# Kernel tuning notes

Hardware: AMD Instinct MI355X
Metric: run time of the kernel (lower is better)

The kernel has to match this reference:

```python
import jax, jax.numpy as jnp
import numpy as np
import math

# Model dims (see shape_source)
BATCH, SEQ, HH, WW = 32, 128, 32, 32   # x: (B, seq_len, H, W); L = H*W = 1024
D_MODEL = 1024                          # hidden_dim
N2 = 4                                  # n=8 -> 4 complex S4D modes
L_MAX = 64                              # SSM kernel length (l_max)


def _layernorm(x, gamma, beta, eps=1e-5):
    mu = jnp.mean(x, axis=-1, keepdims=True)
    var = jnp.var(x, axis=-1, keepdims=True)
    return (x - mu) * jax.lax.rsqrt(var + eps) * gamma + beta


def setup_inputs() -> dict:
    key = jax.random.key(0)
    ks = jax.random.split(key, 12)
    d_in = SEQ  # d_input = d_output = seq_len
    inp = {
        "x": jax.random.normal(ks[0], (BATCH, SEQ, HH, WW), dtype=jnp.float32),
        # encoder Linear(d_input -> d_model)
        "W_enc": jax.random.normal(ks[1], (d_in, D_MODEL), dtype=jnp.float32) / math.sqrt(d_in),
        "b_enc": jnp.zeros((D_MODEL,), dtype=jnp.float32),
        # S4D SSM parameters (per d_model channel, N2 complex modes)
        "log_dt": (jax.random.uniform(ks[2], (D_MODEL,), dtype=jnp.float32)
                   * (math.log(0.1) - math.log(0.001)) + math.log(0.001)),
        "A_log_real": jnp.full((D_MODEL, N2), math.log(0.5), dtype=jnp.float32),
        "A_imag": jnp.broadcast_to(math.pi * jnp.arange(N2, dtype=jnp.float32), (D_MODEL, N2)).copy(),
        "C_real": jax.random.normal(ks[3], (D_MODEL, N2), dtype=jnp.float32) * 0.5,
        "C_imag": jax.random.normal(ks[4], (D_MODEL, N2), dtype=jnp.float32) * 0.5,
        "D": jax.random.normal(ks[5], (D_MODEL,), dtype=jnp.float32),
        # position-wise GLU mixing Linear(d_model -> 2*d_model)
        "W_glu": jax.random.normal(ks[6], (D_MODEL, 2 * D_MODEL), dtype=jnp.float32) / math.sqrt(D_MODEL),
        "b_glu": jnp.zeros((2 * D_MODEL,), dtype=jnp.float32),
        "ln_gamma": jnp.ones((D_MODEL,), dtype=jnp.float32),
        "ln_beta": jnp.zeros((D_MODEL,), dtype=jnp.float32),
        # decoder Linear(d_model -> d_output)
        "W_dec": jax.random.normal(ks[7], (D_MODEL, d_in), dtype=jnp.float32) / math.sqrt(D_MODEL),
        "b_dec": jnp.zeros((d_in,), dtype=jnp.float32),
    }
    return inp


def reference(x, W_enc, b_enc, log_dt, A_log_real, A_imag, C_real, C_imag, D,
              W_glu, b_glu, ln_gamma, ln_beta, W_dec, b_dec):
    Bsz, S, Hh, Ww = x.shape
    L = Hh * Ww
    u = x.reshape(Bsz, S, L)                                  # (B, d_input, L)
    # encoder applied per position along L
    h = jnp.einsum('bdl,de->ble', u, W_enc) + b_enc           # (B, L, d_model)

    # ---- S4D kernel (ZOH discretization, B=1, diagonal A) ----
    dt = jnp.exp(log_dt)                                      # (d,)
    A = -jnp.exp(A_log_real) + 1j * A_imag                    # (d, n2) complex
    Cc = C_real + 1j * C_imag
    dtA = A * dt[:, None]                                     # (d, n2)
    Bd = (jnp.exp(dtA) - 1.0) / A                             # ZOH input matrix
    t = jnp.arange(L_MAX)
    vand = jnp.exp(dtA[:, :, None] * t)                       # (d, n2, l_max)
    K = 2.0 * jnp.einsum('dn,dnl->dl', Cc * Bd, vand).real    # (d, l_max)

    # ---- causal FFT convolution along L + skip D*u ----
    z = jnp.swapaxes(h, 1, 2)                                 # (B, d, L)
    n_fft = L + L_MAX
    y = jnp.fft.irfft(jnp.fft.rfft(z, n=n_fft) * jnp.fft.rfft(K, n=n_fft), n=n_fft)[..., :L]
    y = y + D[:, None] * z                                    # (B, d, L)

    # ---- block: GELU -> GLU mixing -> residual -> LayerNorm ----
    y = jax.nn.gelu(jnp.swapaxes(y, 1, 2))                    # (B, L, d)
    g = y @ W_glu + b_glu                                     # (B, L, 2d)
    g = g[..., :D_MODEL] * jax.nn.sigmoid(g[..., D_MODEL:])
    h = _layernorm(h + g, ln_gamma, ln_beta)                  # (B, L, d)

    out = h @ W_dec + b_dec                                   # (B, L, d_output)
    out = jnp.swapaxes(out, 1, 2).reshape(Bsz, S, Hh, Ww)
    return out
```

## Files before the change

kernel.cpp:

```cpp
#include <hip/hip_runtime.h>
#include <hip/hip_bf16.h>
#include <math.h>

#define B_ 32
#define S_ 128
#define L_ 1024
#define D_ 1024

typedef unsigned short u16;
typedef __attribute__((ext_vector_type(8))) __bf16 bf16x8;
typedef __attribute__((ext_vector_type(4))) float f32x4;

__device__ __forceinline__ float bf2f(u16 u) {
    return __uint_as_float(((unsigned)u) << 16);
}
__device__ __forceinline__ u16 f2bf(float f) {
    unsigned u = __float_as_uint(f);
    u += 0x7FFF + ((u >> 16) & 1);
    return (u16)(u >> 16);
}
__device__ __forceinline__ float gelu_tanh(float x) {
    float x3 = x * x * x;
    float t = tanhf(0.7978845608028654f * (x + 0.044715f * x3));
    return 0.5f * x * (1.0f + t);
}
__device__ __forceinline__ float sigmoidf(float x) {
    return 1.0f / (1.0f + expf(-x));
}
__device__ __forceinline__ void gld16(const void* g, void* l) {
    __builtin_amdgcn_global_load_lds((const __attribute__((address_space(1))) void*)g,
                                     (__attribute__((address_space(3))) void*)l, 16, 0, 0);
}

__global__ __launch_bounds__(256) void k_ssmk(
        const float* __restrict__ log_dt, const float* __restrict__ Alr,
        const float* __restrict__ Aim, const float* __restrict__ Cr,
        const float* __restrict__ Ci, float* __restrict__ Kt) {
    int tid = blockIdx.x * 256 + threadIdx.x;
    int d = tid & (D_ - 1);
    int j = tid >> 10;
    float dt = expf(log_dt[d]);
    float acc = 0.f;
    #pragma unroll
    for (int n = 0; n < 4; ++n) {
        float ar = -expf(Alr[d * 4 + n]);
        float ai = Aim[d * 4 + n];
        float wr = ar * dt, wi = ai * dt;
        float ew = expf(wr);
        float sw, cw; sincosf(wi, &sw, &cw);
        float ur = ew * cw - 1.0f, ui = ew * sw;
        float inv = 1.0f / (ar * ar + ai * ai);
        float bdr = (ur * ar + ui * ai) * inv;
        float bdi = (ui * ar - ur * ai) * inv;
        float cr = Cr[d * 4 + n], ci = Ci[d * 4 + n];
        float cbr = cr * bdr - ci * bdi;
        float cbi = cr * bdi + ci * bdr;
        float ej = expf(wr * (float)j);
        float sj, cj; sincosf(wi * (float)j, &sj, &cj);
        acc += 2.0f * ej * (cbr * cj - cbi * sj);
    }
    Kt[j * D_ + d] = acc;
}

__global__ __launch_bounds__(256) void k_tcast(
        const float* __restrict__ src0, u16* __restrict__ dst0, int R, int C) {
    __shared__ float tile[64][65];
    const float* src = src0 + (size_t)blockIdx.z * R * C;
    u16* dst = dst0 + (size_t)blockIdx.z * R * C;
    int c0 = blockIdx.x * 64;
    int r0 = blockIdx.y * 64;
    int t = threadIdx.x;
    #pragma unroll
    for (int p = 0; p < 4; ++p) {
        int fid = p * 256 + t;
        int rr = fid >> 4, cc = (fid & 15) * 4;
        float4 v = *(const float4*)&src[(size_t)(r0 + rr) * C + c0 + cc];
        tile[rr][cc + 0] = v.x; tile[rr][cc + 1] = v.y;
        tile[rr][cc + 2] = v.z; tile[rr][cc + 3] = v.w;
    }
    __syncthreads();
    #pragma unroll
    for (int p = 0; p < 4; ++p) {
        int fid = p * 256 + t;
        int rr = fid >> 4, cc = (fid & 15) * 4;
        ushort4 o;
        o.x = f2bf(tile[cc + 0][rr]);
        o.y = f2bf(tile[cc + 1][rr]);
        o.z = f2bf(tile[cc + 2][rr]);
        o.w = f2bf(tile[cc + 3][rr]);
        *(ushort4*)&dst[(size_t)(c0 + rr) * R + r0 + cc] = o;
    }
}

__global__ __launch_bounds__(256) void k_enc_mfma(
        const u16* __restrict__ xb, const u16* __restrict__ WeT,
        const float* __restrict__ be, u16* __restrict__ hb) {
    __shared__ u16 As[128 * 128];
    __shared__ u16 Bs[128 * 128];
    int t = threadIdx.x;
    int lane = t & 63, wid = t >> 6;
    int wr = wid & 1, wc = wid >> 1;
    int orig = blockIdx.x;
    int wgid = (orig & 7) * 256 + (orig >> 3);
    int m0 = (wgid >> 3) * 128;
    int e0 = (wgid & 7) * 128;

    #pragma unroll
    for (int c = 0; c < 8; ++c) {
        int ch = wid * 8 + c;
        int r = ch * 4 + (lane >> 4);
        int g = (lane & 15) ^ (r & 15);
        gld16(&xb[(size_t)(m0 + r) * 128 + g * 8], &As[ch * 512]);
        gld16(&WeT[(size_t)(e0 + r) * 128 + g * 8], &Bs[ch * 512]);
    }
    int co4[4];
    #pragma unroll
    for (int kh = 0; kh < 4; ++kh)
        co4[kh] = ((((lane >> 4) + kh * 4) ^ (lane & 15)) * 8);
    int arow[4], brow[4];
    #pragma unroll
    for (int i = 0; i < 4; ++i) arow[i] = (wr * 64 + i * 16 + (lane & 15)) * 128;
    #pragma unroll
    for (int q = 0; q < 4; ++q) brow[q] = (wc * 64 + q * 16 + (lane & 15)) * 128;

    __syncthreads();
    f32x4 acc[4][4] = {};
    #pragma unroll
    for (int kh = 0; kh < 4; ++kh) {
        bf16x8 af[4], bfr[4];
        #pragma unroll
        for (int i = 0; i < 4; ++i) af[i] = *(const bf16x8*)&As[arow[i] + co4[kh]];
        #pragma unroll
        for (int q = 0; q < 4; ++q) bfr[q] = *(const bf16x8*)&Bs[brow[q] + co4[kh]];
        __builtin_amdgcn_s_setprio(1);
        #pragma unroll
        for (int i = 0; i < 4; ++i)
            #pragma unroll
            for (int q = 0; q < 4; ++q)
                acc[i][q] = __builtin_amdgcn_mfma_f32_16x16x32_bf16(af[i], bfr[q], acc[i][q], 0, 0, 0);
        __builtin_amdgcn_s_setprio(0);
    }
    #pragma unroll
    for (int q = 0; q < 4; ++q) {
        int e = e0 + wc * 64 + q * 16 + (lane & 15);
        float bias = be[e];
        #pragma unroll
        for (int i = 0; i < 4; ++i) {
            #pragma unroll
            for (int r = 0; r < 4; ++r) {
                int m = m0 + wr * 64 + i * 16 + (lane >> 4) * 4 + r;
                hb[(size_t)m * 1024 + e] = f2bf(acc[i][q][r] + bias);
            }
        }
    }
}

__global__ __launch_bounds__(256) void k_conv(
        const u16* __restrict__ hb, const float* __restrict__ Kt,
        const float* __restrict__ Dv, u16* __restrict__ yg) {
    __shared__ float hs[128][64];
    int b = blockIdx.z;
    int l0 = blockIdx.y * 64;
    int d0 = blockIdx.x * 64;
    int t = threadIdx.x;
    int dl = t & 63, lg = t >> 6;
    #pragma unroll
    for (int p = 0; p < 8; ++p) {
        int fid = p * 256 + t;
        int r = fid >> 4, c4 = fid & 15;
        int l = l0 - 64 + r;
        float4 v = make_float4(0.f, 0.f, 0.f, 0.f);
        if (l >= 0) {
            ushort4 u = *(const ushort4*)&hb[((size_t)b * 1024 + l) * 1024 + d0 + c4 * 4];
            v = make_float4(bf2f(u.x), bf2f(u.y), bf2f(u.z), bf2f(u.w));
        }
        *(float4*)&hs[r][c4 * 4] = v;
    }
    float kr[64];
    #pragma unroll
    for (int j = 0; j < 64; ++j) kr[j] = Kt[j * 1024 + d0 + dl];
    float Dd = Dv[d0 + dl];
    __syncthreads();
    float acc[16] = {};
    int rbase = lg * 16 + 1;
    #pragma unroll
    for (int s = 0; s < 15; ++s) {
        float hv = hs[rbase + s][dl];
        #pragma unroll
        for (int i = 0; i <= 14; ++i)
            if (i <= s) acc[i] = fmaf(kr[i + 63 - s], hv, acc[i]);
    }
    #pragma unroll
    for (int s = 15; s < 64; ++s) {
        float hv = hs[rbase + s][dl];
        #pragma unroll
        for (int i = 0; i < 16; ++i)
            acc[i] = fmaf(kr[i + 63 - s], hv, acc[i]);
    }
    #pragma unroll
    for (int s = 64; s < 79; ++s) {
        float hv = hs[rbase + s][dl];
        #pragma unroll
        for (int i = 1; i < 16; ++i)
            if (i >= s - 63) acc[i] = fmaf(kr[i + 63 - s], hv, acc[i]);
    }
    #pragma unroll
    for (int i = 0; i < 16; ++i) {
        int l = l0 + lg * 16 + i;
        float z = hs[64 + lg * 16 + i][dl];
        float y = acc[i] + Dd * z;
        yg[((size_t)b * 1024 + l) * 1024 + d0 + dl] = f2bf(gelu_tanh(y));
    }
}

__global__ __launch_bounds__(512, 2) void k_glu256(
        const u16* __restrict__ yg, const u16* __restrict__ WgT,
        const float* __restrict__ bg, u16* __restrict__ hb) {
    __shared__ u16 Asm[2][16384];
    __shared__ u16 Bsm[2][16384];
    int t = threadIdx.x;
    int lane = t & 63, wid = t >> 6;
    int wr = wid >> 2, wc = wid & 3;

    int orig = blockIdx.x;
    int wgid = (orig & 7) * 128 + (orig >> 3);
    int m0 = (wgid >> 3) * 256;
    int p0g = (wgid & 7) * 128;

    int rl = lane >> 3;
    int gsw = ((lane & 7) ^ rl) * 8;
    int ch0 = wid * 2, ch1 = wid * 2 + 1;
    int rA0 = (ch0 >> 3) * 128 + (ch0 & 7) * 8 + rl;
    int rA1 = (ch1 >> 3) * 128 + (ch1 & 7) * 8 + rl;
    int dA0 = ((ch0 >> 3) * 128 + (ch0 & 7) * 8) * 64;
    int dA1 = ((ch1 >> 3) * 128 + (ch1 & 7) * 8) * 64;
    int rB0 = (ch0 >> 2) * 64 + (ch0 & 3) * 8 + rl;
    int rB1 = (ch1 >> 2) * 64 + (ch1 & 3) * 8 + rl;
    int dB0 = ((ch0 >> 2) * 64 + (ch0 & 3) * 8) * 64;
    int dB1 = ((ch1 >> 2) * 64 + (ch1 & 3) * 8) * 64;
    int gB0 = ((rB0 >> 4) & 1) * 1024 + p0g + (((rB0 >> 5) << 4) | (rB0 & 15));
    int gB1 = ((rB1 >> 4) & 1) * 1024 + p0g + (((rB1 >> 5) << 4) | (rB1 & 15));

    int co0 = (((lane >> 4) + 0) ^ (lane & 7)) * 8;
    int co1 = (((lane >> 4) + 4) ^ (lane & 7)) * 8;
    int abase = (wr * 128 + (lane & 15)) * 64;
    int bbase = (wc * 64 + (lane & 15)) * 64;

#define STG_A0(BUF, K0) { gld16(&yg[(size_t)(m0 + rA0) * 1024 + (K0) + gsw], &Asm[BUF][dA0]); \
                          gld16(&yg[(size_t)(m0 + rA1) * 1024 + (K0) + gsw], &Asm[BUF][dA1]); }
#define STG_A1(BUF, K0) { gld16(&yg[(size_t)(m0 + rA0 + 64) * 1024 + (K0) + gsw], &Asm[BUF][dA0 + 4096]); \
                          gld16(&yg[(size_t)(m0 + rA1 + 64) * 1024 + (K0) + gsw], &Asm[BUF][dA1 + 4096]); }
#define STG_B0(BUF, K0) { gld16(&WgT[(size_t)gB0 * 1024 + (K0) + gsw], &Bsm[BUF][dB0]); \
                          gld16(&WgT[(size_t)gB1 * 1024 + (K0) + gsw], &Bsm[BUF][dB1]); }
#define STG_B1(BUF, K0) { gld16(&WgT[(size_t)(gB0 + 16) * 1024 + (K0) + gsw], &Bsm[BUF][dB0 + 2048]); \
                          gld16(&WgT[(size_t)(gB1 + 16) * 1024 + (K0) + gsw], &Bsm[BUF][dB1 + 2048]); }
#define RD_A(MH) { _Pragma("unroll") for (int i = 0; i < 4; ++i) { \
        a0[i][0] = *(const bf16x8*)&Ac[abase + (MH) * 4096 + i * 1024 + co0]; \
        a0[i][1] = *(const bf16x8*)&Ac[abase + (MH) * 4096 + i * 1024 + co1]; } }
#define RD_B(BB, OFS) { _Pragma("unroll") for (int q = 0; q < 2; ++q) { \
        BB[q][0] = *(const bf16x8*)&Bc[bbase + (OFS) + q * 1024 + co0]; \
        BB[q][1] = *(const bf16x8*)&Bc[bbase + (OFS) + q * 1024 + co1]; } }
#define MFMA_CL(MI, BB, NQ) { __builtin_amdgcn_s_setprio(1); \
    _Pragma("unroll") for (int i = 0; i < 4; ++i) \
        _Pragma("unroll") for (int q = 0; q < 2; ++q) { \
            acc[(MI) * 4 + i][(NQ) + q] = __builtin_amdgcn_mfma_f32_16x16x32_bf16(a0[i][0], BB[q][0], acc[(MI) * 4 + i][(NQ) + q], 0, 0, 0); \
            acc[(MI) * 4 + i][(NQ) + q] = __builtin_amdgcn_mfma_f32_16x16x32_bf16(a0[i][1], BB[q][1], acc[(MI) * 4 + i][(NQ) + q], 0, 0, 0); } \
    __builtin_amdgcn_s_setprio(0); }

    f32x4 acc[8][4] = {};
    bf16x8 a0[4][2], b0[2][2], b1[2][2];

    STG_A0(0, 0); STG_B0(0, 0); STG_B1(0, 0); STG_A1(0, 0);

    int cur = 0;
    for (int kt = 0; kt < 15; ++kt) {
        const u16* Ac = &Asm[cur][0];
        const u16* Bc = &Bsm[cur][0];
        int nxt = cur ^ 1, k1 = (kt + 1) * 64;
        asm volatile("s_waitcnt vmcnt(2)" ::: "memory");
        __builtin_amdgcn_s_barrier();
        RD_A(0); RD_B(b0, 0);
        STG_A0(nxt, k1);
        __builtin_amdgcn_s_barrier();
        MFMA_CL(0, b0, 0);
        RD_B(b1, 2048);
        STG_B0(nxt, k1);
        __builtin_amdgcn_s_barrier();
        MFMA_CL(0, b1, 2);
        asm volatile("s_waitcnt vmcnt(4)" ::: "memory");
        __builtin_amdgcn_s_barrier();
        RD_A(1);
        STG_B1(nxt, k1);
        __builtin_amdgcn_s_barrier();
        MFMA_CL(1, b0, 0);
        STG_A1(nxt, k1);
        __builtin_amdgcn_s_barrier();
        MFMA_CL(1, b1, 2);
        cur = nxt;
    }
    {
        const u16* Ac = &Asm[cur][0];
        const u16* Bc = &Bsm[cur][0];
        asm volatile("s_waitcnt vmcnt(2)" ::: "memory");
        __builtin_amdgcn_s_barrier();
        RD_A(0); RD_B(b0, 0);
        MFMA_CL(0, b0, 0);
        RD_B(b1, 2048);
        MFMA_CL(0, b1, 2);
        asm volatile("s_waitcnt vmcnt(0)" ::: "memory");
        __builtin_amdgcn_s_barrier();
        RD_A(1);
        MFMA_CL(1, b0, 0);
        MFMA_CL(1, b1, 2);
    }
    #pragma unroll
    for (int i = 0; i < 8; ++i) {
        #pragma unroll
        for (int tt = 0; tt < 2; ++tt) {
            int col = p0g + (wc * 2 + tt) * 16 + (lane & 15);
            float b1v = bg[col];
            float b2v = bg[1024 + col];
            #pragma unroll
            for (int r = 0; r < 4; ++r) {
                int m = m0 + wr * 128 + i * 16 + (lane >> 4) * 4 + r;
                size_t idx = (size_t)m * 1024 + col;
                float g1 = acc[i][tt * 2][r] + b1v;
                float g2 = acc[i][tt * 2 + 1][r] + b2v;
                hb[idx] = f2bf(bf2f(hb[idx]) + g1 * sigmoidf(g2));
            }
        }
    }
#undef STG_A0
#undef STG_A1
#undef STG_B0
#undef STG_B1
#undef RD_A
#undef RD_B
#undef MFMA_CL
}

__global__ __launch_bounds__(256) void k_ln(
        u16* __restrict__ hb, const float* __restrict__ gamma,
        const float* __restrict__ beta) {
    int row = blockIdx.x;
    int t = threadIdx.x;
    size_t base = (size_t)row * 1024;
    ushort4 u = *(const ushort4*)&hb[base + t * 4];
    float v0 = bf2f(u.x), v1 = bf2f(u.y), v2 = bf2f(u.z), v3 = bf2f(u.w);
    float s = v0 + v1 + v2 + v3;
    float s2 = v0 * v0 + v1 * v1 + v2 * v2 + v3 * v3;
    #pragma unroll
    for (int off = 32; off > 0; off >>= 1) {
        s += __shfl_down(s, off);
        s2 += __shfl_down(s2, off);
    }
    __shared__ float rs[4], rs2[4];
    int wid = t >> 6, lane = t & 63;
    if (lane == 0) { rs[wid] = s; rs2[wid] = s2; }
    __syncthreads();
    float ts = rs[0] + rs[1] + rs[2] + rs[3];
    float ts2 = rs2[0] + rs2[1] + rs2[2] + rs2[3];
    float mean = ts * (1.0f / 1024.0f);
    float var = ts2 * (1.0f / 1024.0f) - mean * mean;
    float rstd = rsqrtf(var + 1e-5f);
    float4 gm = *(const float4*)&gamma[t * 4];
    float4 bt = *(const float4*)&beta[t * 4];
    ushort4 o;
    o.x = f2bf((v0 - mean) * rstd * gm.x + bt.x);
    o.y = f2bf((v1 - mean) * rstd * gm.y + bt.y);
    o.z = f2bf((v2 - mean) * rstd * gm.z + bt.z);
    o.w = f2bf((v3 - mean) * rstd * gm.w + bt.w);
    *(ushort4*)&hb[base + t * 4] = o;
}

__global__ __launch_bounds__(256) void k_dec_mfma(
        const u16* __restrict__ hb, const u16* __restrict__ WdT,
        const float* __restrict__ bd, float* __restrict__ out) {
    __shared__ __align__(16) char smem[65536];
    u16* As = (u16*)smem;
    u16* Bs = (u16*)(smem + 32768);
    float* Ts = (float*)smem;
    int t = threadIdx.x;
    int lane = t & 63, wid = t >> 6;
    int wr = wid & 1, wc = wid >> 1;
    int m0 = blockIdx.x * 128;
    int bb = m0 >> 10, l0 = m0 & 1023;

    int gsrc = (((lane & 7) ^ (lane >> 3)) * 8);
    int rr4[4];
    #pragma unroll
    for (int c = 0; c < 4; ++c) rr4[c] = (wid * 4 + c) * 8 + (lane >> 3);
    int co[2];
    co[0] = (((lane >> 4) + 0) ^ (lane & 7)) * 8;
    co[1] = (((lane >> 4) + 4) ^ (lane & 7)) * 8;
    int arow[4], brow[4];
    #pragma unroll
    for (int i = 0; i < 4; ++i) arow[i] = (wr * 64 + i * 16 + (lane & 15)) * 64;
    #pragma unroll
    for (int q = 0; q < 4; ++q) brow[q] = (wc * 64 + q * 16 + (lane & 15)) * 64;

    f32x4 acc[4][4] = {};
    #pragma unroll
    for (int c = 0; c < 4; ++c) {
        int ch = wid * 4 + c;
        gld16(&hb[(size_t)(m0 + rr4[c]) * 1024 + gsrc], &As[0 * 8192 + ch * 512]);
        gld16(&WdT[(size_t)rr4[c] * 1024 + gsrc], &Bs[0 * 8192 + ch * 512]);
    }
    __syncthreads();
    int cur = 0;
    for (int kt = 0; kt < 16; ++kt) {
        if (kt < 15) {
            int k0 = (kt + 1) * 64;
            #pragma unroll
            for (int c = 0; c < 4; ++c) {
                int ch = wid * 4 + c;
                gld16(&hb[(size_t)(m0 + rr4[c]) * 1024 + k0 + gsrc], &As[(cur ^ 1) * 8192 + ch * 512]);
                gld16(&WdT[(size_t)rr4[c] * 1024 + k0 + gsrc], &Bs[(cur ^ 1) * 8192 + ch * 512]);
            }
        }
        #pragma unroll
        for (int kh = 0; kh < 2; ++kh) {
            bf16x8 af[4], bfr[4];
            #pragma unroll
            for (int i = 0; i < 4; ++i) af[i] = *(const bf16x8*)&As[cur * 8192 + arow[i] + co[kh]];
            #pragma unroll
            for (int q = 0; q < 4; ++q) bfr[q] = *(const bf16x8*)&Bs[cur * 8192 + brow[q] + co[kh]];
            __builtin_amdgcn_s_setprio(1);
            #pragma unroll
            for (int i = 0; i < 4; ++i)
                #pragma unroll
                for (int q = 0; q < 4; ++q)
                    acc[i][q] = __builtin_amdgcn_mfma_f32_16x16x32_bf16(af[i], bfr[q], acc[i][q], 0, 0, 0);
            __builtin_amdgcn_s_setprio(0);
        }
        __syncthreads();
        cur ^= 1;
    }
    __syncthreads();
    #pragma unroll
    for (int ro = 0; ro < 2; ++ro) {
        if (wc == ro) {
            #pragma unroll
            for (int i = 0; i < 4; ++i)
                #pragma unroll
                for (int q = 0; q < 4; ++q) {
                    int sl = q * 16 + (lane & 15);
                    float bias = bd[ro * 64 + sl];
                    #pragma unroll
                    for (int r = 0; r < 4; ++r) {
                        int ml = wr * 64 + i * 16 + (lane >> 4) * 4 + r;
                        Ts[sl * 132 + ml] = acc[i][q][r] + bias;
                    }
                }
        }
        __syncthreads();
        #pragma unroll
        for (int p = 0; p < 8; ++p) {
            int fid = p * 256 + t;
            int sl = fid >> 5, c = (fid & 31) * 4;
            float4 v = *(const float4*)&Ts[sl * 132 + c];
            *(float4*)&out[(size_t)bb * 131072 + (size_t)(ro * 64 + sl) * 1024 + l0 + c] = v;
        }
        __syncthreads();
    }
}

extern "C" void kernel_launch(void* const* d_in, const int* in_sizes, int n_in,
                              void* d_out, int out_size, void* d_ws, size_t ws_size,
                              hipStream_t stream) {
    (void)in_sizes; (void)n_in; (void)out_size; (void)ws_size;
    const float* x   = (const float*)d_in[0];
    const float* We  = (const float*)d_in[1];
    const float* be  = (const float*)d_in[2];
    const float* ldt = (const float*)d_in[3];
    const float* Alr = (const float*)d_in[4];
    const float* Aim = (const float*)d_in[5];
    const float* Cr  = (const float*)d_in[6];
    const float* Ci  = (const float*)d_in[7];
    const float* Dv  = (const float*)d_in[8];
    const float* Wg  = (const float*)d_in[9];
    const float* bg  = (const float*)d_in[10];
    const float* gam = (const float*)d_in[11];
    const float* bet = (const float*)d_in[12];
    const float* Wd  = (const float*)d_in[13];
    const float* bd  = (const float*)d_in[14];
    float* out = (float*)d_out;

    u16* hb = (u16*)d_ws;
    u16* yg = hb + 33554432ull;
    float* Kt = (float*)(yg + 33554432ull);
    u16* WgT = (u16*)(Kt + 65536);
    u16* WdT = WgT + 2097152ull;
    u16* WeT = WdT + 131072ull;
    u16* xb  = yg;

    k_tcast<<<dim3(32, 16, 1), 256, 0, stream>>>(Wg, WgT, 1024, 2048);
    k_tcast<<<dim3(2, 16, 1), 256, 0, stream>>>(Wd, WdT, 1024, 128);
    k_tcast<<<dim3(16, 2, 1), 256, 0, stream>>>(We, WeT, 128, 1024);
    k_tcast<<<dim3(16, 2, 32), 256, 0, stream>>>(x, xb, 128, 1024);
    k_ssmk<<<256, 256, 0, stream>>>(ldt, Alr, Aim, Cr, Ci, Kt);
    k_enc_mfma<<<2048, 256, 0, stream>>>(xb, WeT, be, hb);
    k_conv<<<dim3(16, 16, 32), 256, 0, stream>>>(hb, Kt, Dv, yg);
    k_glu256<<<1024, 512, 0, stream>>>(yg, WgT, bg, hb);
    k_ln<<<32768, 256, 0, stream>>>(hb, gam, bet);
    k_dec_mfma<<<256, 256, 0, stream>>>(hb, WdT, bd, out);
}
```

Baseline: 343.8 us.

## Restructure GLU GEMM mainloop into a 4-stage K=32 LDS pipeline

```diff
diff --git a/kernel.cpp b/kernel.cpp
--- a/kernel.cpp
+++ b/kernel.cpp
@@ -216,8 +216,8 @@
 __global__ __launch_bounds__(512, 2) void k_glu256(
         const u16* __restrict__ yg, const u16* __restrict__ WgT,
         const float* __restrict__ bg, u16* __restrict__ hb) {
-    __shared__ u16 Asm[2][16384];
-    __shared__ u16 Bsm[2][16384];
+    __shared__ u16 Asm[4][8192];
+    __shared__ u16 Bsm[4][8192];
     int t = threadIdx.x;
     int lane = t & 63, wid = t >> 6;
     int wr = wid >> 2, wc = wid & 3;
@@ -227,92 +227,60 @@
     int m0 = (wgid >> 3) * 256;
     int p0g = (wgid & 7) * 128;
 
-    int rl = lane >> 3;
-    int gsw = ((lane & 7) ^ rl) * 8;
-    int ch0 = wid * 2, ch1 = wid * 2 + 1;
-    int rA0 = (ch0 >> 3) * 128 + (ch0 & 7) * 8 + rl;
-    int rA1 = (ch1 >> 3) * 128 + (ch1 & 7) * 8 + rl;
-    int dA0 = ((ch0 >> 3) * 128 + (ch0 & 7) * 8) * 64;
-    int dA1 = ((ch1 >> 3) * 128 + (ch1 & 7) * 8) * 64;
-    int rB0 = (ch0 >> 2) * 64 + (ch0 & 3) * 8 + rl;
-    int rB1 = (ch1 >> 2) * 64 + (ch1 & 3) * 8 + rl;
-    int dB0 = ((ch0 >> 2) * 64 + (ch0 & 3) * 8) * 64;
-    int dB1 = ((ch1 >> 2) * 64 + (ch1 & 3) * 8) * 64;
-    int gB0 = ((rB0 >> 4) & 1) * 1024 + p0g + (((rB0 >> 5) << 4) | (rB0 & 15));
-    int gB1 = ((rB1 >> 4) & 1) * 1024 + p0g + (((rB1 >> 5) << 4) | (rB1 & 15));
-
-    int co0 = (((lane >> 4) + 0) ^ (lane & 7)) * 8;
-    int co1 = (((lane >> 4) + 4) ^ (lane & 7)) * 8;
-    int abase = (wr * 128 + (lane & 15)) * 64;
-    int bbase = (wc * 64 + (lane & 15)) * 64;
-
-#define STG_A0(BUF, K0) { gld16(&yg[(size_t)(m0 + rA0) * 1024 + (K0) + gsw], &Asm[BUF][dA0]); \
-                          gld16(&yg[(size_t)(m0 + rA1) * 1024 + (K0) + gsw], &Asm[BUF][dA1]); }
-#define STG_A1(BUF, K0) { gld16(&yg[(size_t)(m0 + rA0 + 64) * 1024 + (K0) + gsw], &Asm[BUF][dA0 + 4096]); \
-                          gld16(&yg[(size_t)(m0 + rA1 + 64) * 1024 + (K0) + gsw], &Asm[BUF][dA1 + 4096]); }
-#define STG_B0(BUF, K0) { gld16(&WgT[(size_t)gB0 * 1024 + (K0) + gsw], &Bsm[BUF][dB0]); \
-                          gld16(&WgT[(size_t)gB1 * 1024 + (K0) + gsw], &Bsm[BUF][dB1]); }
-#define STG_B1(BUF, K0) { gld16(&WgT[(size_t)(gB0 + 16) * 1024 + (K0) + gsw], &Bsm[BUF][dB0 + 2048]); \
-                          gld16(&WgT[(size_t)(gB1 + 16) * 1024 + (K0) + gsw], &Bsm[BUF][dB1 + 2048]); }
-#define RD_A(MH) { _Pragma("unroll") for (int i = 0; i < 4; ++i) { \
-        a0[i][0] = *(const bf16x8*)&Ac[abase + (MH) * 4096 + i * 1024 + co0]; \
-        a0[i][1] = *(const bf16x8*)&Ac[abase + (MH) * 4096 + i * 1024 + co1]; } }
-#define RD_B(BB, OFS) { _Pragma("unroll") for (int q = 0; q < 2; ++q) { \
-        BB[q][0] = *(const bf16x8*)&Bc[bbase + (OFS) + q * 1024 + co0]; \
-        BB[q][1] = *(const bf16x8*)&Bc[bbase + (OFS) + q * 1024 + co1]; } }
-#define MFMA_CL(MI, BB, NQ) { __builtin_amdgcn_s_setprio(1); \
+    int crow = lane >> 2;
+    int gofs = (((lane & 3) ^ ((lane >> 3) & 3)) * 8);
+    int ch0 = wid * 2, ch1 = ch0 + 1;
+    int rA0 = ch0 * 16 + crow, rA1 = ch1 * 16 + crow;
+    int dA0 = ch0 * 512, dA1 = ch1 * 512;
+    int gB0 = ((rA0 >> 4) & 1) * 1024 + p0g + (((rA0 >> 5) << 4) | (rA0 & 15));
+    int gB1 = ((rA1 >> 4) & 1) * 1024 + p0g + (((rA1 >> 5) << 4) | (rA1 & 15));
+
+    int aco = (lane & 15) * 32 + (((lane >> 4) ^ (((lane & 15) >> 1) & 3)) * 8);
+    int abase = wr * 128 * 32;
+    int bbase = wc * 64 * 32;
+
+#define STAGE_A(T) { int k0_ = (T) * 32; u16* d_ = &Asm[(T) & 3][0]; \
+    gld16(&yg[(size_t)(m0 + rA0) * 1024 + k0_ + gofs], d_ + dA0); \
+    gld16(&yg[(size_t)(m0 + rA1) * 1024 + k0_ + gofs], d_ + dA1); }
+#define STAGE_B(T) { int k0_ = (T) * 32; u16* d_ = &Bsm[(T) & 3][0]; \
+    gld16(&WgT[(size_t)gB0 * 1024 + k0_ + gofs], d_ + dA0); \
+    gld16(&WgT[(size_t)gB1 * 1024 + k0_ + gofs], d_ + dA1); }
+
+    f32x4 acc[8][4] = {};
+    bf16x8 af[4], bf[4];
+
+    STAGE_A(0); STAGE_B(0); STAGE_A(1); STAGE_B(1); STAGE_A(2); STAGE_B(2);
+
+#define TILE_BODY(KT, WAITN, DO_STAGE) { \
+    asm volatile("s_waitcnt vmcnt(" #WAITN ")" ::: "memory"); \
+    __builtin_amdgcn_s_barrier(); \
+    __builtin_amdgcn_sched_barrier(0); \
+    const u16* Ac_ = &Asm[(KT) & 3][0]; \
+    const u16* Bc_ = &Bsm[(KT) & 3][0]; \
+    _Pragma("unroll") for (int q = 0; q < 4; ++q) bf[q] = *(const bf16x8*)&Bc_[bbase + q * 512 + aco]; \
+    _Pragma("unroll") for (int i = 0; i < 4; ++i) af[i] = *(const bf16x8*)&Ac_[abase + i * 512 + aco]; \
+    if (DO_STAGE) STAGE_A((KT) + 3); \
+    __builtin_amdgcn_s_setprio(1); \
     _Pragma("unroll") for (int i = 0; i < 4; ++i) \
-        _Pragma("unroll") for (int q = 0; q < 2; ++q) { \
-            acc[(MI) * 4 + i][(NQ) + q] = __builtin_amdgcn_mfma_f32_16x16x32_bf16(a0[i][0], BB[q][0], acc[(MI) * 4 + i][(NQ) + q], 0, 0, 0); \
-            acc[(MI) * 4 + i][(NQ) + q] = __builtin_amdgcn_mfma_f32_16x16x32_bf16(a0[i][1], BB[q][1], acc[(MI) * 4 + i][(NQ) + q], 0, 0, 0); } \
+        _Pragma("unroll") for (int q = 0; q < 4; ++q) \
+            acc[i][q] = __builtin_amdgcn_mfma_f32_16x16x32_bf16(af[i], bf[q], acc[i][q], 0, 0, 0); \
+    __builtin_amdgcn_s_setprio(0); \
+    _Pragma("unroll") for (int i = 0; i < 4; ++i) af[i] = *(const bf16x8*)&Ac_[abase + 2048 + i * 512 + aco]; \
+    if (DO_STAGE) STAGE_B((KT) + 3); \
+    __builtin_amdgcn_s_setprio(1); \
+    _Pragma("unroll") for (int i = 0; i < 4; ++i) \
+        _Pragma("unroll") for (int q = 0; q < 4; ++q) \
+            acc[4 + i][q] = __builtin_amdgcn_mfma_f32_16x16x32_bf16(af[i], bf[q], acc[4 + i][q], 0, 0, 0); \
     __builtin_amdgcn_s_setprio(0); }
 
-    f32x4 acc[8][4] = {};
-    bf16x8 a0[4][2], b0[2][2], b1[2][2];
-
-    STG_A0(0, 0); STG_B0(0, 0); STG_B1(0, 0); STG_A1(0, 0);
-
-    int cur = 0;
-    for (int kt = 0; kt < 15; ++kt) {
-        const u16* Ac = &Asm[cur][0];
-        const u16* Bc = &Bsm[cur][0];
-        int nxt = cur ^ 1, k1 = (kt + 1) * 64;
-        asm volatile("s_waitcnt vmcnt(2)" ::: "memory");
-        __builtin_amdgcn_s_barrier();
-        RD_A(0); RD_B(b0, 0);
-        STG_A0(nxt, k1);
-        __builtin_amdgcn_s_barrier();
-        MFMA_CL(0, b0, 0);
-        RD_B(b1, 2048);
-        STG_B0(nxt, k1);
-        __builtin_amdgcn_s_barrier();
-        MFMA_CL(0, b1, 2);
-        asm volatile("s_waitcnt vmcnt(4)" ::: "memory");
-        __builtin_amdgcn_s_barrier();
-        RD_A(1);
-        STG_B1(nxt, k1);
-        __builtin_amdgcn_s_barrier();
-        MFMA_CL(1, b0, 0);
-        STG_A1(nxt, k1);
-        __builtin_amdgcn_s_barrier();
-        MFMA_CL(1, b1, 2);
-        cur = nxt;
-    }
-    {
-        const u16* Ac = &Asm[cur][0];
-        const u16* Bc = &Bsm[cur][0];
-        asm volatile("s_waitcnt vmcnt(2)" ::: "memory");
-        __builtin_amdgcn_s_barrier();
-        RD_A(0); RD_B(b0, 0);
-        MFMA_CL(0, b0, 0);
-        RD_B(b1, 2048);
-        MFMA_CL(0, b1, 2);
-        asm volatile("s_waitcnt vmcnt(0)" ::: "memory");
-        __builtin_amdgcn_s_barrier();
-        RD_A(1);
-        MFMA_CL(1, b0, 0);
-        MFMA_CL(1, b1, 2);
-    }
+    for (int kt = 0; kt < 29; ++kt) TILE_BODY(kt, 8, 1);
+    TILE_BODY(29, 8, 0);
+    TILE_BODY(30, 4, 0);
+    TILE_BODY(31, 0, 0);
+#undef TILE_BODY
+#undef STAGE_A
+#undef STAGE_B
+
     #pragma unroll
     for (int i = 0; i < 8; ++i) {
         #pragma unroll
@@ -330,13 +298,6 @@
             }
         }
     }
-#undef STG_A0
-#undef STG_A1
-#undef STG_B0
-#undef STG_B1
-#undef RD_A
-#undef RD_B
-#undef MFMA_CL
 }
 
 __global__ __launch_bounds__(256) void k_ln(
```

New measurement: 349.6 us. Within noise of the previous version (+1.7%).
